# Kernel optimization log

Hardware: AMD Instinct MI355X
Metric: run time of the kernel (lower is better)

The kernel has to match this reference:

```python
import jax, jax.numpy as jnp
import numpy as np

BATCH, NUM_FRAMES, FFT_SIZE = 256, 256, 512

def setup_inputs() -> dict:
    key = jax.random.key(0)
    k1, k2 = jax.random.split(key)
    inputs = jax.random.normal(k1, (BATCH, NUM_FRAMES, FFT_SIZE), dtype=jnp.float32)
    # Hann-like window (cfg.win_fn is a fixed per-bin window of length fft_size)
    window_fn = (0.5 - 0.5 * jnp.cos(2.0 * jnp.pi * jnp.arange(FFT_SIZE, dtype=jnp.float32) / FFT_SIZE))
    return {"inputs": inputs, "window_fn": window_fn}

def reference(inputs, window_fn):
    # window each frame, FFT along last axis (norm='backward' is jnp default), keep real part
    spec = jnp.fft.fft(inputs * window_fn, axis=-1).real.astype(jnp.float32)
    # output shape (batch, num_frames, fft_size, 1) as in the original reshape
    return spec[..., None]
```

## Files before the change

kernel.cpp:

```cpp
#include <hip/hip_runtime.h>
#include <math.h>

#define FFT_N 512
#define WAVES_PER_BLOCK 4
#define LDS_STRIDE 576

#define WAVE_LDS_SYNC() do { \
    __builtin_amdgcn_wave_barrier(); \
    asm volatile("s_waitcnt lgkmcnt(0)" ::: "memory"); \
    __builtin_amdgcn_wave_barrier(); \
} while (0)

__device__ __forceinline__ void fft8(float* re, float* im) {
    const float C = 0.70710678118654752440f;
    float tr[8], ti[8];
    tr[0]=re[0]+re[4]; ti[0]=im[0]+im[4];
    tr[4]=re[0]-re[4]; ti[4]=im[0]-im[4];
    tr[1]=re[1]+re[5]; ti[1]=im[1]+im[5];
    tr[5]=re[1]-re[5]; ti[5]=im[1]-im[5];
    tr[2]=re[2]+re[6]; ti[2]=im[2]+im[6];
    tr[6]=re[2]-re[6]; ti[6]=im[2]-im[6];
    tr[3]=re[3]+re[7]; ti[3]=im[3]+im[7];
    tr[7]=re[3]-re[7]; ti[7]=im[3]-im[7];
    { float a=tr[5], b=ti[5]; tr[5]=C*(a+b); ti[5]=C*(b-a); }
    { float a=tr[6], b=ti[6]; tr[6]=b;       ti[6]=-a;      }
    { float a=tr[7], b=ti[7]; tr[7]=C*(b-a); ti[7]=-C*(a+b);}
    {
        float s0r=tr[0]+tr[2], s0i=ti[0]+ti[2];
        float s2r=tr[0]-tr[2], s2i=ti[0]-ti[2];
        float s1r=tr[1]+tr[3], s1i=ti[1]+ti[3];
        float dr =tr[1]-tr[3], di =ti[1]-ti[3];
        float s3r= di, s3i=-dr;
        re[0]=s0r+s1r; im[0]=s0i+s1i;
        re[2]=s2r+s3r; im[2]=s2i+s3i;
        re[4]=s0r-s1r; im[4]=s0i-s1i;
        re[6]=s2r-s3r; im[6]=s2i-s3i;
    }
    {
        float s0r=tr[4]+tr[6], s0i=ti[4]+ti[6];
        float s2r=tr[4]-tr[6], s2i=ti[4]-ti[6];
        float s1r=tr[5]+tr[7], s1i=ti[5]+ti[7];
        float dr =tr[5]-tr[7], di =ti[5]-ti[7];
        float s3r= di, s3i=-dr;
        re[1]=s0r+s1r; im[1]=s0i+s1i;
        re[3]=s2r+s3r; im[3]=s2i+s3i;
        re[5]=s0r-s1r; im[5]=s0i-s1i;
        re[7]=s2r-s3r; im[7]=s2i-s3i;
    }
}

__device__ __forceinline__ void twiddle_chain(float* re, float* im,
                                              float c, float s) {
    float cr = c, ci = s;
#pragma unroll
    for (int k = 1; k < 8; ++k) {
        float a = re[k], b = im[k];
        re[k] = a * cr - b * ci;
        im[k] = a * ci + b * cr;
        float ncr = cr * c - ci * s;
        float nci = cr * s + ci * c;
        cr = ncr; ci = nci;
    }
}

__global__ __launch_bounds__(256) void fft512_pack2_kernel(
        const float* __restrict__ x,
        const float* __restrict__ win,
        float* __restrict__ out) {
    __shared__ float2 lds[WAVES_PER_BLOCK * LDS_STRIDE];

    const int wave = threadIdx.x >> 6;
    const int lane = threadIdx.x & 63;
    const int pair = blockIdx.x * WAVES_PER_BLOCK + wave;
    float2* __restrict__ L = lds + wave * LDS_STRIDE;

    const float* __restrict__ x0 = x + (size_t)(2 * pair) * FFT_N;
    const float* __restrict__ x1 = x0 + FFT_N;

    float re[8], im[8];

#pragma unroll
    for (int n1 = 0; n1 < 8; ++n1) {
        const int idx = lane + 64 * n1;
        const float w = win[idx];
        re[n1] = x0[idx] * w;
        im[n1] = x1[idx] * w;
    }

    fft8(re, im);
    {
        float s, c;
        __sincosf(-6.283185307179586f * (float)lane * (1.0f / 512.0f), &s, &c);
        twiddle_chain(re, im, c, s);
    }

#pragma unroll
    for (int k1 = 0; k1 < 8; ++k1)
        L[k1 * 72 + lane] = make_float2(re[k1], im[k1]);
    WAVE_LDS_SYNC();
    const int k1p = lane >> 3, n3p = lane & 7;
#pragma unroll
    for (int n2 = 0; n2 < 8; ++n2) {
        float2 v = L[k1p * 72 + n2 * 8 + n3p];
        re[n2] = v.x; im[n2] = v.y;
    }
    WAVE_LDS_SYNC();

    fft8(re, im);
    {
        float s, c;
        __sincosf(-6.283185307179586f * (float)n3p * (1.0f / 64.0f), &s, &c);
        twiddle_chain(re, im, c, s);
    }

#pragma unroll
    for (int k2 = 0; k2 < 8; ++k2)
        L[(k1p * 8 + k2) * 9 + n3p] = make_float2(re[k2], im[k2]);
    WAVE_LDS_SYNC();
    const int k1pp = lane & 7, k2pp = lane >> 3;
#pragma unroll
    for (int n3 = 0; n3 < 8; ++n3) {
        float2 v = L[(k1pp * 8 + k2pp) * 9 + n3];
        re[n3] = v.x; im[n3] = v.y;
    }
    WAVE_LDS_SYNC();

    fft8(re, im);

#pragma unroll
    for (int k3 = 0; k3 < 8; ++k3)
        L[k3 * 72 + lane] = make_float2(re[k3], im[k3]);
    WAVE_LDS_SYNC();

    float* __restrict__ o0 = out + (size_t)(2 * pair) * FFT_N;
    float* __restrict__ o1 = o0 + FFT_N;
#pragma unroll
    for (int k3 = 0; k3 < 8; ++k3) {
        const int k  = lane + 64 * k3;
        const int kk = (FFT_N - k) & (FFT_N - 1);
        float2 p = L[(kk >> 6) * 72 + (kk & 63)];
        o0[k] = 0.5f * (re[k3] + p.x);
        o1[k] = 0.5f * (im[k3] + p.y);
    }
}

extern "C" void kernel_launch(void* const* d_in, const int* in_sizes, int n_in,
                              void* d_out, int out_size, void* d_ws, size_t ws_size,
                              hipStream_t stream) {
    const float* x   = (const float*)d_in[0];
    const float* win = (const float*)d_in[1];
    float* out       = (float*)d_out;

    const int rows   = in_sizes[0] / FFT_N;
    const int pairs  = rows / 2;
    const int blocks = pairs / WAVES_PER_BLOCK;
    hipLaunchKernelGGL(fft512_pack2_kernel, dim3(blocks), dim3(256), 0, stream,
                       x, win, out);
}
```

Before: 228.7 us.

## Vectorize global IO via swizzled LDS staging and process two pairs per wave with prefetch

Replaces the strided scalar global loads and stores with float4 accesses, staging data through LDS with XOR and bit-permutation swizzles so the FFT stages still see the layouts they expect. Each wave now handles two row pairs and prefetches the next pair's input while the current one is transformed. Twiddle sincos values and the swizzle indices are computed once and reused across both pairs. This adds extra LDS round trips and barriers per pair, and halves the block count, which lowers available parallelism.

Result: no change. 229.7 us (+0.4%).

```diff
diff --git a/kernel.cpp b/kernel.cpp
--- a/kernel.cpp
+++ b/kernel.cpp
@@ -3,6 +3,7 @@
 
 #define FFT_N 512
 #define WAVES_PER_BLOCK 4
+#define PAIRS_PER_WAVE 2
 #define LDS_STRIDE 576
 
 #define WAVE_LDS_SYNC() do { \
@@ -63,6 +64,13 @@
     }
 }
 
+__device__ __forceinline__ int swz3(int m) {
+    return ((m ^ (m >> 2)) & 1)
+         | (((m >> 3) & 7) << 1)
+         | (((m >> 1) & 1) << 4)
+         | (((m >> 2) & 1) << 5);
+}
+
 __global__ __launch_bounds__(256) void fft512_pack2_kernel(
         const float* __restrict__ x,
         const float* __restrict__ win,
@@ -71,76 +79,135 @@
 
     const int wave = threadIdx.x >> 6;
     const int lane = threadIdx.x & 63;
-    const int pair = blockIdx.x * WAVES_PER_BLOCK + wave;
     float2* __restrict__ L = lds + wave * LDS_STRIDE;
 
-    const float* __restrict__ x0 = x + (size_t)(2 * pair) * FFT_N;
-    const float* __restrict__ x1 = x0 + FFT_N;
-
-    float re[8], im[8];
-
-#pragma unroll
-    for (int n1 = 0; n1 < 8; ++n1) {
-        const int idx = lane + 64 * n1;
-        const float w = win[idx];
-        re[n1] = x0[idx] * w;
-        im[n1] = x1[idx] * w;
-    }
-
-    fft8(re, im);
-    {
-        float s, c;
-        __sincosf(-6.283185307179586f * (float)lane * (1.0f / 512.0f), &s, &c);
-        twiddle_chain(re, im, c, s);
-    }
-
-#pragma unroll
-    for (int k1 = 0; k1 < 8; ++k1)
-        L[k1 * 72 + lane] = make_float2(re[k1], im[k1]);
-    WAVE_LDS_SYNC();
-    const int k1p = lane >> 3, n3p = lane & 7;
-#pragma unroll
-    for (int n2 = 0; n2 < 8; ++n2) {
-        float2 v = L[k1p * 72 + n2 * 8 + n3p];
-        re[n2] = v.x; im[n2] = v.y;
-    }
-    WAVE_LDS_SYNC();
-
-    fft8(re, im);
-    {
-        float s, c;
-        __sincosf(-6.283185307179586f * (float)n3p * (1.0f / 64.0f), &s, &c);
-        twiddle_chain(re, im, c, s);
-    }
-
-#pragma unroll
-    for (int k2 = 0; k2 < 8; ++k2)
-        L[(k1p * 8 + k2) * 9 + n3p] = make_float2(re[k2], im[k2]);
-    WAVE_LDS_SYNC();
-    const int k1pp = lane & 7, k2pp = lane >> 3;
-#pragma unroll
-    for (int n3 = 0; n3 < 8; ++n3) {
-        float2 v = L[(k1pp * 8 + k2pp) * 9 + n3];
-        re[n3] = v.x; im[n3] = v.y;
-    }
-    WAVE_LDS_SYNC();
-
-    fft8(re, im);
-
-#pragma unroll
-    for (int k3 = 0; k3 < 8; ++k3)
-        L[k3 * 72 + lane] = make_float2(re[k3], im[k3]);
-    WAVE_LDS_SYNC();
-
-    float* __restrict__ o0 = out + (size_t)(2 * pair) * FFT_N;
-    float* __restrict__ o1 = o0 + FFT_N;
-#pragma unroll
-    for (int k3 = 0; k3 < 8; ++k3) {
-        const int k  = lane + 64 * k3;
-        const int kk = (FFT_N - k) & (FFT_N - 1);
-        float2 p = L[(kk >> 6) * 72 + (kk & 63)];
-        o0[k] = 0.5f * (re[k3] + p.x);
-        o1[k] = 0.5f * (im[k3] + p.y);
+    const int t4   = lane << 2;
+    const int u    = lane & 15;
+    const int pp   = lane >> 4;
+    const int x0sw = (lane >> 2) & 3;
+    const int l0r  = lane ^ pp;
+    const int k1p  = lane >> 3;
+    const int n3p  = lane & 7;
+    const int rl   = (lane >> 3) | ((lane & 7) << 3);
+    const int s3w  = swz3(rl);
+
+    int sm[4], smm[4];
+#pragma unroll
+    for (int j = 0; j < 4; ++j) {
+        const int m = 4 * u + j;
+        sm[j]  = swz3(m);
+        smm[j] = swz3((64 - m) & 63);
+    }
+
+    float cA, sA, cB, sB;
+    __sincosf(-6.283185307179586f * (float)lane * (1.0f / 512.0f), &sA, &cA);
+    __sincosf(-6.283185307179586f * (float)n3p  * (1.0f / 64.0f),  &sB, &cB);
+
+    const int pair0 = (blockIdx.x * WAVES_PER_BLOCK + wave) * PAIRS_PER_WAVE;
+
+    const float4 w0 = *(const float4*)(win + t4);
+    const float4 w1 = *(const float4*)(win + t4 + 256);
+
+    const float* __restrict__ xp0 = x + (size_t)(2 * pair0) * FFT_N;
+    float4 ca0 = *(const float4*)(xp0 + t4);
+    float4 cb0 = *(const float4*)(xp0 + FFT_N + t4);
+    float4 ca1 = *(const float4*)(xp0 + t4 + 256);
+    float4 cb1 = *(const float4*)(xp0 + FFT_N + t4 + 256);
+
+#pragma unroll
+    for (int p = 0; p < PAIRS_PER_WAVE; ++p) {
+        {
+            const float* a0 = (const float*)&ca0;
+            const float* b0 = (const float*)&cb0;
+            const float* a1 = (const float*)&ca1;
+            const float* b1 = (const float*)&cb1;
+            const float* W0 = (const float*)&w0;
+            const float* W1 = (const float*)&w1;
+#pragma unroll
+            for (int j = 0; j < 4; ++j) {
+                L[t4 +       (j ^ x0sw)] = make_float2(a0[j] * W0[j], b0[j] * W0[j]);
+                L[t4 + 256 + (j ^ x0sw)] = make_float2(a1[j] * W1[j], b1[j] * W1[j]);
+            }
+        }
+        WAVE_LDS_SYNC();
+
+        float4 na0, nb0, na1, nb1;
+        if (p + 1 < PAIRS_PER_WAVE) {
+            const float* __restrict__ np = x + (size_t)(2 * (pair0 + p + 1)) * FFT_N;
+            na0 = *(const float4*)(np + t4);
+            nb0 = *(const float4*)(np + FFT_N + t4);
+            na1 = *(const float4*)(np + t4 + 256);
+            nb1 = *(const float4*)(np + FFT_N + t4 + 256);
+        } else {
+            na0 = ca0; nb0 = cb0; na1 = ca1; nb1 = cb1;
+        }
+
+        float re[8], im[8];
+#pragma unroll
+        for (int n1 = 0; n1 < 8; ++n1) {
+            float2 v = L[n1 * 64 + l0r];
+            re[n1] = v.x; im[n1] = v.y;
+        }
+        WAVE_LDS_SYNC();
+
+        fft8(re, im);
+        twiddle_chain(re, im, cA, sA);
+
+#pragma unroll
+        for (int k1 = 0; k1 < 8; ++k1)
+            L[k1 * 72 + lane] = make_float2(re[k1], im[k1]);
+        WAVE_LDS_SYNC();
+#pragma unroll
+        for (int n2 = 0; n2 < 8; ++n2) {
+            float2 v = L[k1p * 72 + n2 * 8 + n3p];
+            re[n2] = v.x; im[n2] = v.y;
+        }
+        WAVE_LDS_SYNC();
+
+        fft8(re, im);
+        twiddle_chain(re, im, cB, sB);
+
+#pragma unroll
+        for (int k2 = 0; k2 < 8; ++k2)
+            L[(k1p * 8 + k2) * 9 + n3p] = make_float2(re[k2], im[k2]);
+        WAVE_LDS_SYNC();
+#pragma unroll
+        for (int n3 = 0; n3 < 8; ++n3) {
+            float2 v = L[lane * 9 + n3];
+            re[n3] = v.x; im[n3] = v.y;
+        }
+        WAVE_LDS_SYNC();
+
+        fft8(re, im);
+
+#pragma unroll
+        for (int k3 = 0; k3 < 8; ++k3)
+            L[(k3 << 6) + s3w] = make_float2(re[k3], im[k3]);
+        WAVE_LDS_SYNC();
+
+        float* __restrict__ o0 = out + (size_t)(2 * (pair0 + p)) * FFT_N;
+        float* __restrict__ o1 = o0 + FFT_N;
+#pragma unroll
+        for (int half = 0; half < 2; ++half) {
+            const int hk = 4 * half + pp;
+            float4 ra, rb;
+            float* pa = (float*)&ra;
+            float* pb = (float*)&rb;
+#pragma unroll
+            for (int j = 0; j < 4; ++j) {
+                const int m  = 4 * u + j;
+                const int hn = ((512 - (hk << 6) - m) >> 6) & 7;
+                const float2 zk = L[(hk << 6) + sm[j]];
+                const float2 zn = L[(hn << 6) + smm[j]];
+                pa[j] = 0.5f * (zk.x + zn.x);
+                pb[j] = 0.5f * (zk.y + zn.y);
+            }
+            *(float4*)(o0 + 256 * half + t4) = ra;
+            *(float4*)(o1 + 256 * half + t4) = rb;
+        }
+        WAVE_LDS_SYNC();
+
+        ca0 = na0; cb0 = nb0; ca1 = na1; cb1 = nb1;
     }
 }
 
@@ -153,7 +220,7 @@
 
     const int rows   = in_sizes[0] / FFT_N;
     const int pairs  = rows / 2;
-    const int blocks = pairs / WAVES_PER_BLOCK;
+    const int blocks = pairs / (WAVES_PER_BLOCK * PAIRS_PER_WAVE);
     hipLaunchKernelGGL(fft512_pack2_kernel, dim3(blocks), dim3(256), 0, stream,
                        x, win, out);
 }
```
